# Kernel optimization log

Measured on AMD Instinct MI355X. Metric: run time of the kernel, lower is better.

The kernel has to match this reference:

```python
import jax, jax.numpy as jnp
import numpy as np


def _conv1x1(x, w, b):
    # x: (B,C,H,W), w: (O,C), b: (O,)
    return jnp.einsum('oc,bchw->bohw', w, x) + b[None, :, None, None]


def _avg_pool2(x):
    B, C, H, W = x.shape
    return x.reshape(B, C, H // 2, 2, W // 2, 2).mean(axis=(3, 5))


def setup_inputs() -> dict:
    key = jax.random.key(0)
    B, C, H, W = 8, 64, 64, 64
    ks = jax.random.split(key, 14)
    s = 1.0 / np.sqrt(C)

    def wb(k1, k2):
        return (jax.random.uniform(k1, (C, C), jnp.float32, -s, s),
                jax.random.uniform(k2, (C,), jnp.float32, -s, s))

    w_q, b_q = wb(ks[0], ks[1])
    w_K, b_K = wb(ks[2], ks[3])
    w_V, b_V = wb(ks[4], ks[5])
    w_Q, b_Q = wb(ks[6], ks[7])
    w_k, b_k = wb(ks[8], ks[9])
    w_v, b_v = wb(ks[10], ks[11])
    x = jax.random.normal(ks[12], (B, C, H, W), jnp.float32)
    gamma = jnp.ones((1,), jnp.float32)
    return dict(x=x, w_q=w_q, b_q=b_q, w_K=w_K, b_K=b_K, w_V=w_V, b_V=b_V,
                w_Q=w_Q, b_Q=b_Q, w_k=w_k, b_k=b_k, w_v=w_v, b_v=b_v,
                gamma=gamma)


def reference(x, w_q, b_q, w_K, b_K, w_V, b_V, w_Q, b_Q, w_k, b_k, w_v, b_v, gamma):
    B, C, H, W = x.shape
    N = H * W
    N4 = N // 4

    # Stage 1: pooled queries vs full key/value
    q = _conv1x1(x, w_q, b_q)                      # (B,C,H,W); torch views as (B,C,W,H) but H==W
    qp = _avg_pool2(q).reshape(B, C, N4).transpose(0, 2, 1)   # (B,N/4,C)
    Kf = _conv1x1(x, w_K, b_K).reshape(B, C, N)                # (B,C,N)
    Vf = _conv1x1(x, w_V, b_V).reshape(B, C, N)                # (B,C,N)
    attn = jax.nn.softmax(jnp.einsum('bnc,bcm->bnm', qp, Kf), axis=-1)  # (B,N/4,N)
    out = jnp.einsum('bcm,bnm->bcn', Vf, attn)                 # (B,C,N/4)
    out = out.reshape(B, C, H // 2, W // 2)

    # Stage 2: full queries vs pooled-derived key/value
    Qf = _conv1x1(x, w_Q, b_Q).reshape(B, C, N).transpose(0, 2, 1)  # (B,N,C)
    kp = _conv1x1(out, w_k, b_k).reshape(B, C, N4)                  # (B,C,N/4)
    vp = _conv1x1(out, w_v, b_v).reshape(B, C, N4)                  # (B,C,N/4)
    attn2 = jax.nn.softmax(jnp.einsum('bnc,bcm->bnm', Qf, kp), axis=-1)  # (B,N,N/4)
    out2 = jnp.einsum('bcm,bnm->bcn', vp, attn2).reshape(B, C, H, W)

    return gamma * out2 + x
```

## Files before the change

kernel.cpp:

```cpp
#include <hip/hip_runtime.h>
#include <math.h>


typedef __bf16 bf16;
typedef __attribute__((ext_vector_type(4))) __bf16 bf16x4;
typedef __attribute__((ext_vector_type(8))) __bf16 bf16x8;
typedef __attribute__((ext_vector_type(4))) float f32x4;

constexpr float LOG2E = 1.4426950408889634f;

__device__ __forceinline__ void gl_lds16(const bf16* g, bf16* l) {
    __builtin_amdgcn_global_load_lds(
        (const __attribute__((address_space(1))) unsigned int*)g,
        (__attribute__((address_space(3))) unsigned int*)l,
        16, 0, 0);
}

__device__ __forceinline__ float vexp2(float x) {
    float r;
    asm("v_exp_f32 %0, %1" : "=v"(r) : "v"(x));
    return r;
}
__device__ __forceinline__ unsigned cvtpk(float a, float b) {
    unsigned r;
    asm("v_cvt_pk_bf16_f32 %0, %1, %2" : "=v"(r) : "v"(a), "v"(b));
    return r;
}
__device__ __forceinline__ void swap32(unsigned &a, unsigned &b) {
    asm("v_permlane32_swap_b32 %0, %1" : "+v"(a), "+v"(b));
}
__device__ __forceinline__ void swap16(unsigned &a, unsigned &b) {
    asm("v_permlane16_swap_b32 %0, %1" : "+v"(a), "+v"(b));
}

struct WFrag { bf16x8 f[4][2]; };

template<int WT>
__device__ __forceinline__ WFrag load_wfrag(const float* __restrict__ W, int lane,
                                            float sc = 1.0f) {
    const int c16 = lane & 15, q4 = lane >> 4;
    WFrag wf;
    #pragma unroll
    for (int to = 0; to < 4; ++to)
        #pragma unroll
        for (int h = 0; h < 2; ++h) {
            bf16 tmp[8];
            if (WT == 0) {
                const float* wp = W + (16 * to + c16) * 64 + q4 * 8 + 32 * h;
                float4 f0 = *(const float4*)wp;
                float4 f1 = *(const float4*)(wp + 4);
                tmp[0] = (bf16)(f0.x * sc); tmp[1] = (bf16)(f0.y * sc);
                tmp[2] = (bf16)(f0.z * sc); tmp[3] = (bf16)(f0.w * sc);
                tmp[4] = (bf16)(f1.x * sc); tmp[5] = (bf16)(f1.y * sc);
                tmp[6] = (bf16)(f1.z * sc); tmp[7] = (bf16)(f1.w * sc);
            } else {
                #pragma unroll
                for (int j = 0; j < 8; ++j)
                    tmp[j] = (bf16)(W[(q4 * 8 + 32 * h + j) * 64 + 16 * to + c16] * sc);
            }
            wf.f[to][h] = *(bf16x8*)tmp;
        }
    return wf;
}

template<int OUT>
__device__ __forceinline__ void proj_run(
    const bf16* __restrict__ src, int TN, const WFrag& wf, const float* __restrict__ Bs,
    bf16* __restrict__ Y, int N, int b, int gn0, bf16* __restrict__ Yl, int lane)
{
    const int c16 = lane & 15, q4 = lane >> 4;
    for (int tn = 0; tn < TN; ++tn) {
        bf16x8 xb0 = *(const bf16x8*)&src[(16 * tn + c16) * 72 + q4 * 8];
        bf16x8 xb1 = *(const bf16x8*)&src[(16 * tn + c16) * 72 + q4 * 8 + 32];
        #pragma unroll
        for (int to = 0; to < 4; ++to) {
            f32x4 acc = (f32x4){0.f, 0.f, 0.f, 0.f};
            acc = __builtin_amdgcn_mfma_f32_16x16x32_bf16(wf.f[to][0], xb0, acc, 0, 0, 0);
            acc = __builtin_amdgcn_mfma_f32_16x16x32_bf16(wf.f[to][1], xb1, acc, 0, 0, 0);
            float bias[4] = {0.f, 0.f, 0.f, 0.f};
            if (Bs) {
                float4 b4 = *(const float4*)(Bs + 16 * to + q4 * 4);
                bias[0] = b4.x; bias[1] = b4.y; bias[2] = b4.z; bias[3] = b4.w;
            }
            if (OUT == 0) {
                bf16x4 yv;
                #pragma unroll
                for (int r = 0; r < 4; ++r) yv[r] = (bf16)(acc[r] + bias[r]);
                *(bf16x4*)(Y + ((size_t)b * N + gn0 + 16 * tn + c16) * 64 + 16 * to + 4 * q4) = yv;
            } else if (OUT == 1) {
                #pragma unroll
                for (int r = 0; r < 4; ++r)
                    Y[((size_t)b * 64 + 16 * to + 4 * q4 + r) * N + gn0 + 16 * tn + c16] =
                        (bf16)(acc[r] + bias[r]);
            } else {
                bf16x4 yv;
                #pragma unroll
                for (int r = 0; r < 4; ++r) yv[r] = (bf16)(acc[r] + bias[r]);
                *(bf16x4*)&Yl[(16 * tn + c16) * 72 + 16 * to + 4 * q4] = yv;
            }
        }
    }
}

__global__ __launch_bounds__(256) void prep_kernel(
    const float* __restrict__ x,
    const float* __restrict__ w_q, const float* __restrict__ b_q,
    const float* __restrict__ w_K,
    bf16* __restrict__ xt, bf16* __restrict__ xn, bf16* __restrict__ qkt)
{
    __shared__ float tile[128 * 65];
    __shared__ __align__(16) bf16 xpb[32 * 72];
    __shared__ __align__(16) bf16 qtile[32 * 72];
    const int t  = threadIdx.x;
    const int h2 = blockIdx.x;
    const int b  = blockIdx.y;
    const int n0 = h2 * 128;

    #pragma unroll
    for (int i = 0; i < 32; ++i) {
        int lin = i * 256 + t;
        int n = lin & 127, c = lin >> 7;
        tile[n * 65 + c] = x[((size_t)b * 64 + c) * 4096 + n0 + n];
    }
    __syncthreads();
    {
        int wp = t & 31, c0 = (t >> 5) * 8;
        bf16 tmp[8];
        #pragma unroll
        for (int j = 0; j < 8; ++j) {
            float a = tile[(2 * wp) * 65 + c0 + j] + tile[(2 * wp + 1) * 65 + c0 + j]
                    + tile[(64 + 2 * wp) * 65 + c0 + j] + tile[(64 + 2 * wp + 1) * 65 + c0 + j];
            tmp[j] = (bf16)(0.25f * a);
        }
        *(bf16x8*)&xpb[wp * 72 + c0] = *(bf16x8*)tmp;
    }
    __syncthreads();

    #pragma unroll
    for (int i = 0; i < 4; ++i) {
        int slot = i * 256 + t;
        int n = slot >> 3, c0 = (slot & 7) * 8;
        bf16 tmp[8];
        #pragma unroll
        for (int j = 0; j < 8; ++j) tmp[j] = (bf16)tile[n * 65 + c0 + j];
        *(bf16x8*)&xt[((size_t)b * 4096 + n0 + n) * 64 + c0] = *(bf16x8*)tmp;
    }
    #pragma unroll
    for (int i = 0; i < 4; ++i) {
        int slot = i * 256 + t;
        int c = slot >> 4, n8 = slot & 15;
        bf16 tmp[8];
        #pragma unroll
        for (int j = 0; j < 8; ++j) tmp[j] = (bf16)tile[(n8 * 8 + j) * 65 + c];
        *(bf16x8*)&xn[((size_t)b * 64 + c) * 4096 + n0 + n8 * 8] = *(bf16x8*)tmp;
    }
    if ((t >> 6) == 3) {
        const int lane = t & 63;
        WFrag wfq  = load_wfrag<0>(w_q, lane);
        WFrag wfKT = load_wfrag<1>(w_K, lane, LOG2E);
        proj_run<2>(xpb, 2, wfq, b_q, nullptr, 0, 0, 0, qtile, lane);
        asm volatile("s_waitcnt lgkmcnt(0)" ::: "memory");
        proj_run<0>(qtile, 2, wfKT, nullptr, qkt, 1024, b, h2 * 32, nullptr, lane);
    }
}

template<int NSPLIT, int MODE, int U, int KS, bool BIAS>
__global__ __launch_bounds__(256 * KS, KS == 1 ? 3 : 2) void flash_kernel(
    const bf16* __restrict__ Qt, const bf16* __restrict__ Kt,
    const bf16* __restrict__ Vn, int NQ, int L,
    bf16* __restrict__ Opart, float* __restrict__ Lbuf,
    float* __restrict__ out_f, const float* __restrict__ resid,
    const float* __restrict__ gamma_p, const float* __restrict__ Gb)
{
    const int tid  = threadIdx.x;
    const int lane = tid & 63;
    const int w    = tid >> 6;
    const int wl   = w & 3;
    const int g    = w >> 2;
    const int c16  = lane & 15;
    const int q4   = lane >> 4;
    const int b    = blockIdx.y;
    const int n0   = blockIdx.x * (64 * U) + wl * (16 * U);
    const int s    = (NSPLIT > 1) ? blockIdx.z : 0;
    const int SL   = L / (NSPLIT * KS);
    const int k0   = (s * KS + g) * SL;
    const int ntiles = SL / 64;

    __shared__ __align__(16) char smem[(size_t)KS * 2 * 4096 * 2 * 2];
    bf16* Ksm = (bf16*)smem;
    bf16* Vsm = (bf16*)(smem + (size_t)KS * 2 * 4096 * 2);

    const int rl8 = lane >> 3;
    const int cg  = ((lane & 7) - rl8) & 7;

    const bf16* Kb = Kt + (size_t)b * L * 64;
    const bf16* Vb = Vn + (size_t)b * 64 * L;

    bf16x8 bq[U][2];
    #pragma unroll
    for (int u = 0; u < U; ++u) {
        const bf16* qrow = Qt + ((size_t)b * NQ + n0 + 16 * u + c16) * 64 + q4 * 8;
        bq[u][0] = *(const bf16x8*)(qrow);
        bq[u][1] = *(const bf16x8*)(qrow + 32);
    }

    f32x4 O[U][4];
    #pragma unroll
    for (int u = 0; u < U; ++u)
        #pragma unroll
        for (int gi = 0; gi < 4; ++gi) O[u][gi] = (f32x4){0.f, 0.f, 0.f, 0.f};
    float l_acc[U];
    #pragma unroll
    for (int u = 0; u < U; ++u) l_acc[u] = 0.f;

    #pragma unroll
    for (int j = 0; j < 2; ++j) {
        const int row = 16 * wl + 8 * j + rl8;
        gl_lds16(Kb + (size_t)(k0 + row) * 64 + cg * 8, &Ksm[(g * 2 + 0) * 4096 + (16 * wl + 8 * j) * 64]);
        gl_lds16(Vb + (size_t)row * L + k0 + cg * 8,    &Vsm[(g * 2 + 0) * 4096 + (16 * wl + 8 * j) * 64]);
    }
    __syncthreads();

    for (int it = 0; it < ntiles; ++it) {
        const int buf = it & 1;
        if (it + 1 < ntiles) {
            const int kn = k0 + (it + 1) * 64;
            #pragma unroll
            for (int j = 0; j < 2; ++j) {
                const int row = 16 * wl + 8 * j + rl8;
                gl_lds16(Kb + (size_t)(kn + row) * 64 + cg * 8,
                         &Ksm[(g * 2 + (buf ^ 1)) * 4096 + (16 * wl + 8 * j) * 64]);
                gl_lds16(Vb + (size_t)row * L + kn + cg * 8,
                         &Vsm[(g * 2 + (buf ^ 1)) * 4096 + (16 * wl + 8 * j) * 64]);
            }
        }

        f32x4 sv[U][4];
        #pragma unroll
        for (int t = 0; t < 4; ++t) {
            const bf16* krow = &Ksm[(g * 2 + buf) * 4096 + (16 * t + c16) * 64];
            bf16x8 ak0 = *(const bf16x8*)&krow[((q4 + c16) & 7) * 8];
            bf16x8 ak1 = *(const bf16x8*)&krow[((q4 + 4 + c16) & 7) * 8];
            #pragma unroll
            for (int u = 0; u < U; ++u) {
                f32x4 z = (f32x4){0.f, 0.f, 0.f, 0.f};
                z = __builtin_amdgcn_mfma_f32_16x16x32_bf16(ak0, bq[u][0], z, 0, 0, 0);
                sv[u][t] = __builtin_amdgcn_mfma_f32_16x16x32_bf16(ak1, bq[u][1], z, 0, 0, 0);
            }
        }

        float4 gb[4];
        if (BIAS) {
            #pragma unroll
            for (int t = 0; t < 4; ++t)
                gb[t] = *(const float4*)&Gb[(size_t)b * 1024 + k0 + it * 64 + 16 * t + 4 * q4];
        }

        bf16x8 pfs[U][2];
        #pragma unroll
        for (int u = 0; u < U; ++u) {
            #pragma unroll
            for (int t = 0; t < 4; ++t)
                #pragma unroll
                for (int r = 0; r < 4; ++r) {
                    float sval = sv[u][t][r];
                    if (BIAS) sval += ((const float*)&gb[t])[r];
                    float p = vexp2(sval);
                    sv[u][t][r] = p;
                    l_acc[u] += p;
                }
            unsigned A0 = cvtpk(sv[u][0][0], sv[u][0][1]);
            unsigned A1 = cvtpk(sv[u][0][2], sv[u][0][3]);
            unsigned A2 = cvtpk(sv[u][2][0], sv[u][2][1]);
            unsigned A3 = cvtpk(sv[u][2][2], sv[u][2][3]);
            unsigned B0 = cvtpk(sv[u][1][0], sv[u][1][1]);
            unsigned B1 = cvtpk(sv[u][1][2], sv[u][1][3]);
            unsigned B2 = cvtpk(sv[u][3][0], sv[u][3][1]);
            unsigned B3 = cvtpk(sv[u][3][2], sv[u][3][3]);
            swap32(A0, B0); swap16(A0, B0);
            swap32(A1, B1); swap16(A1, B1);
            swap32(A2, B2); swap16(A2, B2);
            swap32(A3, B3); swap16(A3, B3);
            union { unsigned wd[4]; bf16x8 v; } p0, p1;
            p0.wd[0] = A0; p0.wd[1] = A1; p0.wd[2] = B0; p0.wd[3] = B1;
            p1.wd[0] = A2; p1.wd[1] = A3; p1.wd[2] = B2; p1.wd[3] = B3;
            pfs[u][0] = p0.v;
            pfs[u][1] = p1.v;
        }

        #pragma unroll
        for (int h = 0; h < 2; ++h) {
            #pragma unroll
            for (int gi = 0; gi < 4; ++gi) {
                bf16x8 av = *(const bf16x8*)&Vsm[(g * 2 + buf) * 4096 +
                                                 (16 * gi + c16) * 64 + ((4 * h + q4 + c16) & 7) * 8];
                #pragma unroll
                for (int u = 0; u < U; ++u)
                    O[u][gi] = __builtin_amdgcn_mfma_f32_16x16x32_bf16(av, pfs[u][h], O[u][gi], 0, 0, 0);
            }
        }
        __syncthreads();
    }

    float l_tot[U];
    #pragma unroll
    for (int u = 0; u < U; ++u) {
        float l = l_acc[u];
        l += __shfl_xor(l, 16);
        l += __shfl_xor(l, 32);
        l_tot[u] = l;
    }

    if (KS == 2) {
        float* sc = (float*)smem;
        const int base = (wl * 64 + lane) * 34;
        if (g == 1) {
            #pragma unroll
            for (int u = 0; u < U; ++u) {
                #pragma unroll
                for (int gi = 0; gi < 4; ++gi)
                    #pragma unroll
                    for (int r = 0; r < 4; ++r)
                        sc[base + u * 16 + gi * 4 + r] = O[u][gi][r];
                sc[base + 32 + u] = l_tot[u];
            }
        }
        __syncthreads();
        if (g == 1) return;
        #pragma unroll
        for (int u = 0; u < U; ++u) {
            #pragma unroll
            for (int gi = 0; gi < 4; ++gi)
                #pragma unroll
                for (int r = 0; r < 4; ++r)
                    O[u][gi][r] += sc[base + u * 16 + gi * 4 + r];
            l_tot[u] += sc[base + 32 + u];
        }
    }

    if (MODE == 2) {
        const float gm = gamma_p[0];
        #pragma unroll
        for (int u = 0; u < U; ++u) {
            float inv = gm / l_tot[u];
            const int n = n0 + 16 * u + c16;
            #pragma unroll
            for (int gi = 0; gi < 4; ++gi) {
                #pragma unroll
                for (int r = 0; r < 4; ++r) {
                    size_t oidx = ((size_t)b * 64 + 16 * gi + 4 * q4 + r) * NQ + n;
                    out_f[oidx] = O[u][gi][r] * inv + resid[oidx];
                }
            }
        }
    } else {
        #pragma unroll
        for (int u = 0; u < U; ++u) {
            float inv = 1.0f / l_tot[u];
            bf16* dst = Opart + ((size_t)(b * NSPLIT + s) * NQ + n0 + 16 * u + c16) * 64 + q4 * 4;
            #pragma unroll
            for (int gi = 0; gi < 4; ++gi) {
                bf16x4 yv;
                #pragma unroll
                for (int r = 0; r < 4; ++r) yv[r] = (bf16)(O[u][gi][r] * inv);
                *(bf16x4*)(dst + 16 * gi) = yv;
            }
        }
        if (lane < 16) {
            #pragma unroll
            for (int u = 0; u < U; ++u)
                Lbuf[(b * NSPLIT + s) * NQ + n0 + 16 * u + lane] = l_tot[u];
        }
    }
}

__global__ __launch_bounds__(256) void comb1kv_kernel(
    const bf16* __restrict__ Opart, const float* __restrict__ Lbuf,
    const float* __restrict__ w_V, const float* __restrict__ b_V,
    const float* __restrict__ w_k, const float* __restrict__ b_k,
    const float* __restrict__ w_v, const float* __restrict__ b_v,
    const float* __restrict__ w_Q, const float* __restrict__ b_Q,
    bf16* __restrict__ qk2t, bf16* __restrict__ vp, float* __restrict__ Gb)
{
    constexpr int NS = 4;
    __shared__ __align__(16) bf16 tile[32 * 72];
    __shared__ __align__(16) bf16 otile[32 * 72];
    __shared__ __align__(16) bf16 kpl[32 * 72];
    __shared__ float wbuf[32 * NS];
    const int t  = threadIdx.x;
    const int m0 = blockIdx.x * 32;
    const int b  = blockIdx.y;
    const int w  = t >> 6;
    const int lane = t & 63;

    WFrag wf;
    if      (w == 0) wf = load_wfrag<0>(w_V, lane);
    else if (w == 1) wf = load_wfrag<0>(w_k, lane);
    else if (w == 2) wf = load_wfrag<0>(w_v, lane);
    else             wf = load_wfrag<1>(w_Q, lane, LOG2E);

    if (t < 32) {
        int m = m0 + t;
        float ls[NS], lt = 0.f;
        #pragma unroll
        for (int s = 0; s < NS; ++s) {
            ls[s] = Lbuf[(b * NS + s) * 1024 + m];
            lt += ls[s];
        }
        float inv = 1.f / lt;
        #pragma unroll
        for (int s = 0; s < NS; ++s) wbuf[t * NS + s] = ls[s] * inv;
    }
    __syncthreads();

    #pragma unroll
    for (int i = 0; i < 2; ++i) {
        int ml = i * 16 + (t >> 4);
        int c4 = (t & 15) * 4;
        const bf16* base = Opart + ((size_t)(b * NS) * 1024 + m0 + ml) * 64 + c4;
        float a0 = 0.f, a1 = 0.f, a2 = 0.f, a3 = 0.f;
        #pragma unroll
        for (int s = 0; s < NS; ++s) {
            bf16x4 v = *(const bf16x4*)(base + (size_t)s * 1024 * 64);
            float wg = wbuf[ml * NS + s];
            a0 += (float)v[0] * wg; a1 += (float)v[1] * wg;
            a2 += (float)v[2] * wg; a3 += (float)v[3] * wg;
        }
        bf16x4 o; o[0] = (bf16)a0; o[1] = (bf16)a1; o[2] = (bf16)a2; o[3] = (bf16)a3;
        *(bf16x4*)&tile[ml * 72 + c4] = o;
    }
    __syncthreads();

    if (w == 0) proj_run<2>(tile, 2, wf, b_V, nullptr, 0, 0, 0, otile, lane);
    __syncthreads();
    if (w == 1) proj_run<2>(otile, 2, wf, b_k, nullptr, 0, 0, 0, kpl, lane);
    if (w == 2) proj_run<1>(otile, 2, wf, b_v, vp, 1024, b, m0, nullptr, lane);
    __syncthreads();
    if (w == 3) proj_run<0>(kpl, 2, wf, nullptr, qk2t, 1024, b, m0, nullptr, lane);
    if (w == 0 && lane < 32) {
        float acc = 0.f;
        #pragma unroll
        for (int c = 0; c < 64; ++c) acc += b_Q[c] * (float)kpl[lane * 72 + c];
        Gb[(size_t)b * 1024 + m0 + lane] = acc * LOG2E;
    }
}

extern "C" void kernel_launch(void* const* d_in, const int* in_sizes, int n_in,
                              void* d_out, int out_size, void* d_ws, size_t ws_size,
                              hipStream_t stream) {
    const float* x    = (const float*)d_in[0];
    const float* w_q  = (const float*)d_in[1];
    const float* b_q  = (const float*)d_in[2];
    const float* w_K  = (const float*)d_in[3];
    const float* b_K  = (const float*)d_in[4];   (void)b_K;
    const float* w_V  = (const float*)d_in[5];
    const float* b_V  = (const float*)d_in[6];
    const float* w_Q  = (const float*)d_in[7];
    const float* b_Q  = (const float*)d_in[8];
    const float* w_k  = (const float*)d_in[9];
    const float* b_k  = (const float*)d_in[10];
    const float* w_v  = (const float*)d_in[11];
    const float* b_v  = (const float*)d_in[12];
    const float* gamma = (const float*)d_in[13];
    float* out = (float*)d_out;

    char* ws = (char*)d_ws;
    bf16*  xt    = (bf16*)ws;   ws += (size_t)8 * 4096 * 64 * 2;
    bf16*  xn    = (bf16*)ws;   ws += (size_t)8 * 4096 * 64 * 2;
    bf16*  qkt   = (bf16*)ws;   ws += (size_t)8 * 1024 * 64 * 2;
    bf16*  qk2t  = (bf16*)ws;   ws += (size_t)8 * 1024 * 64 * 2;
    bf16*  vp    = (bf16*)ws;   ws += (size_t)8 * 64 * 1024 * 2;
    bf16*  Opart = (bf16*)ws;   ws += (size_t)8 * 4 * 1024 * 64 * 2;
    float* Lb    = (float*)ws;  ws += (size_t)8 * 4 * 1024 * 4;
    float* Gb    = (float*)ws;  ws += (size_t)8 * 1024 * 4;

    prep_kernel<<<dim3(32, 8), 256, 0, stream>>>(x, w_q, b_q, w_K, xt, xn, qkt);

    flash_kernel<4, 1, 2, 2, false><<<dim3(8, 8, 4), 512, 0, stream>>>(
        qkt, xt, xn, 1024, 4096, Opart, Lb, nullptr, nullptr, nullptr, nullptr);

    comb1kv_kernel<<<dim3(32, 8), 256, 0, stream>>>(
        Opart, Lb, w_V, b_V, w_k, b_k, w_v, b_v, w_Q, b_Q, qk2t, vp, Gb);

    flash_kernel<1, 2, 2, 2, true><<<dim3(32, 8, 1), 512, 0, stream>>>(
        xt, qk2t, vp, 4096, 1024, nullptr, nullptr, out, x, gamma, Gb);
}
```

Before: 133.4 us.

## Fuse four pipeline kernels into one cooperative persistent kernel with grid syncs

The four launches (prep, first flash attention, combine/projection, second flash attention) are merged into one cooperative kernel of 256 blocks × 512 threads, with grid-wide barriers between phases. Each phase is now a device function working on one shared 64 KB shared-memory buffer, and the prep and combine phases are adapted to the 512-thread block. The aim is to remove per-launch overhead and the idle gaps between dependent kernels. The trade-off is the cost of grid.sync barriers, a single fused register allocation sized for the heaviest phase, and one block per CU.

Result: slower. 229.8 us (+72.3%).

```diff
diff --git a/kernel.cpp b/kernel.cpp
--- a/kernel.cpp
+++ b/kernel.cpp
@@ -1,5 +1,8 @@
 #include <hip/hip_runtime.h>
+#include <hip/hip_cooperative_groups.h>
 #include <math.h>
+
+namespace cg = cooperative_groups;
 
 
 typedef __bf16 bf16;
@@ -102,28 +105,26 @@
     }
 }
 
-__global__ __launch_bounds__(256) void prep_kernel(
+__device__ __forceinline__ void prep_phase(
+    char* smem, int t, int h2, int b,
     const float* __restrict__ x,
     const float* __restrict__ w_q, const float* __restrict__ b_q,
     const float* __restrict__ w_K,
     bf16* __restrict__ xt, bf16* __restrict__ xn, bf16* __restrict__ qkt)
 {
-    __shared__ float tile[128 * 65];
-    __shared__ __align__(16) bf16 xpb[32 * 72];
-    __shared__ __align__(16) bf16 qtile[32 * 72];
-    const int t  = threadIdx.x;
-    const int h2 = blockIdx.x;
-    const int b  = blockIdx.y;
+    float* tile = (float*)smem;
+    bf16* xpb   = (bf16*)(smem + 33280);
+    bf16* qtile = (bf16*)(smem + 37888);
     const int n0 = h2 * 128;
 
     #pragma unroll
-    for (int i = 0; i < 32; ++i) {
-        int lin = i * 256 + t;
+    for (int i = 0; i < 16; ++i) {
+        int lin = i * 512 + t;
         int n = lin & 127, c = lin >> 7;
         tile[n * 65 + c] = x[((size_t)b * 64 + c) * 4096 + n0 + n];
     }
     __syncthreads();
-    {
+    if (t < 256) {
         int wp = t & 31, c0 = (t >> 5) * 8;
         bf16 tmp[8];
         #pragma unroll
@@ -137,8 +138,8 @@
     __syncthreads();
 
     #pragma unroll
-    for (int i = 0; i < 4; ++i) {
-        int slot = i * 256 + t;
+    for (int i = 0; i < 2; ++i) {
+        int slot = i * 512 + t;
         int n = slot >> 3, c0 = (slot & 7) * 8;
         bf16 tmp[8];
         #pragma unroll
@@ -146,8 +147,8 @@
         *(bf16x8*)&xt[((size_t)b * 4096 + n0 + n) * 64 + c0] = *(bf16x8*)tmp;
     }
     #pragma unroll
-    for (int i = 0; i < 4; ++i) {
-        int slot = i * 256 + t;
+    for (int i = 0; i < 2; ++i) {
+        int slot = i * 512 + t;
         int c = slot >> 4, n8 = slot & 15;
         bf16 tmp[8];
         #pragma unroll
@@ -164,31 +165,29 @@
     }
 }
 
-template<int NSPLIT, int MODE, int U, int KS, bool BIAS>
-__global__ __launch_bounds__(256 * KS, KS == 1 ? 3 : 2) void flash_kernel(
+template<int NSPLIT, int MODE, int U, bool BIAS>
+__device__ __forceinline__ void flash_phase(
+    char* smem, int tid, int bx, int b, int s,
     const bf16* __restrict__ Qt, const bf16* __restrict__ Kt,
     const bf16* __restrict__ Vn, int NQ, int L,
     bf16* __restrict__ Opart, float* __restrict__ Lbuf,
     float* __restrict__ out_f, const float* __restrict__ resid,
     const float* __restrict__ gamma_p, const float* __restrict__ Gb)
 {
-    const int tid  = threadIdx.x;
+    constexpr int KS = 2;
     const int lane = tid & 63;
     const int w    = tid >> 6;
     const int wl   = w & 3;
     const int g    = w >> 2;
     const int c16  = lane & 15;
     const int q4   = lane >> 4;
-    const int b    = blockIdx.y;
-    const int n0   = blockIdx.x * (64 * U) + wl * (16 * U);
-    const int s    = (NSPLIT > 1) ? blockIdx.z : 0;
+    const int n0   = bx * (64 * U) + wl * (16 * U);
     const int SL   = L / (NSPLIT * KS);
     const int k0   = (s * KS + g) * SL;
     const int ntiles = SL / 64;
 
-    __shared__ __align__(16) char smem[(size_t)KS * 2 * 4096 * 2 * 2];
     bf16* Ksm = (bf16*)smem;
-    bf16* Vsm = (bf16*)(smem + (size_t)KS * 2 * 4096 * 2);
+    bf16* Vsm = (bf16*)(smem + 32768);
 
     const int rl8 = lane >> 3;
     const int cg  = ((lane & 7) - rl8) & 7;
@@ -311,7 +310,7 @@
         l_tot[u] = l;
     }
 
-    if (KS == 2) {
+    {
         float* sc = (float*)smem;
         const int base = (wl * 64 + lane) * 34;
         if (g == 1) {
@@ -326,55 +325,59 @@
             }
         }
         __syncthreads();
-        if (g == 1) return;
-        #pragma unroll
-        for (int u = 0; u < U; ++u) {
-            #pragma unroll
-            for (int gi = 0; gi < 4; ++gi)
-                #pragma unroll
-                for (int r = 0; r < 4; ++r)
-                    O[u][gi][r] += sc[base + u * 16 + gi * 4 + r];
-            l_tot[u] += sc[base + 32 + u];
-        }
-    }
-
-    if (MODE == 2) {
-        const float gm = gamma_p[0];
-        #pragma unroll
-        for (int u = 0; u < U; ++u) {
-            float inv = gm / l_tot[u];
-            const int n = n0 + 16 * u + c16;
-            #pragma unroll
-            for (int gi = 0; gi < 4; ++gi) {
-                #pragma unroll
-                for (int r = 0; r < 4; ++r) {
-                    size_t oidx = ((size_t)b * 64 + 16 * gi + 4 * q4 + r) * NQ + n;
-                    out_f[oidx] = O[u][gi][r] * inv + resid[oidx];
+        if (g == 0) {
+            #pragma unroll
+            for (int u = 0; u < U; ++u) {
+                #pragma unroll
+                for (int gi = 0; gi < 4; ++gi)
+                    #pragma unroll
+                    for (int r = 0; r < 4; ++r)
+                        O[u][gi][r] += sc[base + u * 16 + gi * 4 + r];
+                l_tot[u] += sc[base + 32 + u];
+            }
+        }
+    }
+
+    if (g == 0) {
+        if (MODE == 2) {
+            const float gm = gamma_p[0];
+            #pragma unroll
+            for (int u = 0; u < U; ++u) {
+                float inv = gm / l_tot[u];
+                const int n = n0 + 16 * u + c16;
+                #pragma unroll
+                for (int gi = 0; gi < 4; ++gi) {
+                    #pragma unroll
+                    for (int r = 0; r < 4; ++r) {
+                        size_t oidx = ((size_t)b * 64 + 16 * gi + 4 * q4 + r) * NQ + n;
+                        out_f[oidx] = O[u][gi][r] * inv + resid[oidx];
+                    }
                 }
             }
-        }
-    } else {
-        #pragma unroll
-        for (int u = 0; u < U; ++u) {
-            float inv = 1.0f / l_tot[u];
-            bf16* dst = Opart + ((size_t)(b * NSPLIT + s) * NQ + n0 + 16 * u + c16) * 64 + q4 * 4;
-            #pragma unroll
-            for (int gi = 0; gi < 4; ++gi) {
-                bf16x4 yv;
-                #pragma unroll
-                for (int r = 0; r < 4; ++r) yv[r] = (bf16)(O[u][gi][r] * inv);
-                *(bf16x4*)(dst + 16 * gi) = yv;
-            }
-        }
-        if (lane < 16) {
-            #pragma unroll
-            for (int u = 0; u < U; ++u)
-                Lbuf[(b * NSPLIT + s) * NQ + n0 + 16 * u + lane] = l_tot[u];
-        }
-    }
-}
-
-__global__ __launch_bounds__(256) void comb1kv_kernel(
+        } else {
+            #pragma unroll
+            for (int u = 0; u < U; ++u) {
+                float inv = 1.0f / l_tot[u];
+                bf16* dst = Opart + ((size_t)(b * NSPLIT + s) * NQ + n0 + 16 * u + c16) * 64 + q4 * 4;
+                #pragma unroll
+                for (int gi = 0; gi < 4; ++gi) {
+                    bf16x4 yv;
+                    #pragma unroll
+                    for (int r = 0; r < 4; ++r) yv[r] = (bf16)(O[u][gi][r] * inv);
+                    *(bf16x4*)(dst + 16 * gi) = yv;
+                }
+            }
+            if (lane < 16) {
+                #pragma unroll
+                for (int u = 0; u < U; ++u)
+                    Lbuf[(b * NSPLIT + s) * NQ + n0 + 16 * u + lane] = l_tot[u];
+            }
+        }
+    }
+}
+
+__device__ __forceinline__ void comb_phase(
+    char* smem, int t, int m0, int b,
     const bf16* __restrict__ Opart, const float* __restrict__ Lbuf,
     const float* __restrict__ w_V, const float* __restrict__ b_V,
     const float* __restrict__ w_k, const float* __restrict__ b_k,
@@ -383,13 +386,10 @@
     bf16* __restrict__ qk2t, bf16* __restrict__ vp, float* __restrict__ Gb)
 {
     constexpr int NS = 4;
-    __shared__ __align__(16) bf16 tile[32 * 72];
-    __shared__ __align__(16) bf16 otile[32 * 72];
-    __shared__ __align__(16) bf16 kpl[32 * 72];
-    __shared__ float wbuf[32 * NS];
-    const int t  = threadIdx.x;
-    const int m0 = blockIdx.x * 32;
-    const int b  = blockIdx.y;
+    bf16* tile  = (bf16*)smem;
+    bf16* otile = (bf16*)(smem + 4608);
+    bf16* kpl   = (bf16*)(smem + 9216);
+    float* wbuf = (float*)(smem + 13824);
     const int w  = t >> 6;
     const int lane = t & 63;
 
@@ -397,7 +397,7 @@
     if      (w == 0) wf = load_wfrag<0>(w_V, lane);
     else if (w == 1) wf = load_wfrag<0>(w_k, lane);
     else if (w == 2) wf = load_wfrag<0>(w_v, lane);
-    else             wf = load_wfrag<1>(w_Q, lane, LOG2E);
+    else if (w == 3) wf = load_wfrag<1>(w_Q, lane, LOG2E);
 
     if (t < 32) {
         int m = m0 + t;
@@ -413,9 +413,8 @@
     }
     __syncthreads();
 
-    #pragma unroll
-    for (int i = 0; i < 2; ++i) {
-        int ml = i * 16 + (t >> 4);
+    {
+        int ml = t >> 4;
         int c4 = (t & 15) * 4;
         const bf16* base = Opart + ((size_t)(b * NS) * 1024 + m0 + ml) * 64 + c4;
         float a0 = 0.f, a1 = 0.f, a2 = 0.f, a3 = 0.f;
@@ -443,6 +442,41 @@
         for (int c = 0; c < 64; ++c) acc += b_Q[c] * (float)kpl[lane * 72 + c];
         Gb[(size_t)b * 1024 + m0 + lane] = acc * LOG2E;
     }
+}
+
+__global__ __launch_bounds__(512, 1) void fused_kernel(
+    const float* __restrict__ x,
+    const float* __restrict__ w_q, const float* __restrict__ b_q,
+    const float* __restrict__ w_K,
+    const float* __restrict__ w_V, const float* __restrict__ b_V,
+    const float* __restrict__ w_Q, const float* __restrict__ b_Q,
+    const float* __restrict__ w_k, const float* __restrict__ b_k,
+    const float* __restrict__ w_v, const float* __restrict__ b_v,
+    const float* __restrict__ gamma_p, float* __restrict__ out,
+    bf16* __restrict__ xt, bf16* __restrict__ xn,
+    bf16* __restrict__ qkt, bf16* __restrict__ qk2t, bf16* __restrict__ vp,
+    bf16* __restrict__ Opart, float* __restrict__ Lb, float* __restrict__ Gb)
+{
+    __shared__ __align__(16) char smem[65536];
+    cg::grid_group grid = cg::this_grid();
+    const int bid = blockIdx.x;
+    const int tid = threadIdx.x;
+
+    prep_phase(smem, tid, bid & 31, bid >> 5, x, w_q, b_q, w_K, xt, xn, qkt);
+    grid.sync();
+
+    flash_phase<4, 1, 2, false>(smem, tid, bid & 7, (bid >> 3) & 7, bid >> 6,
+                                qkt, xt, xn, 1024, 4096,
+                                Opart, Lb, nullptr, nullptr, nullptr, nullptr);
+    grid.sync();
+
+    comb_phase(smem, tid, (bid & 31) * 32, bid >> 5, Opart, Lb,
+               w_V, b_V, w_k, b_k, w_v, b_v, w_Q, b_Q, qk2t, vp, Gb);
+    grid.sync();
+
+    flash_phase<1, 2, 2, true>(smem, tid, bid & 31, bid >> 5, 0,
+                               xt, qk2t, vp, 4096, 1024,
+                               nullptr, nullptr, out, x, gamma_p, Gb);
 }
 
 extern "C" void kernel_launch(void* const* d_in, const int* in_sizes, int n_in,
@@ -474,14 +508,14 @@
     float* Lb    = (float*)ws;  ws += (size_t)8 * 4 * 1024 * 4;
     float* Gb    = (float*)ws;  ws += (size_t)8 * 1024 * 4;
 
-    prep_kernel<<<dim3(32, 8), 256, 0, stream>>>(x, w_q, b_q, w_K, xt, xn, qkt);
-
-    flash_kernel<4, 1, 2, 2, false><<<dim3(8, 8, 4), 512, 0, stream>>>(
-        qkt, xt, xn, 1024, 4096, Opart, Lb, nullptr, nullptr, nullptr, nullptr);
-
-    comb1kv_kernel<<<dim3(32, 8), 256, 0, stream>>>(
-        Opart, Lb, w_V, b_V, w_k, b_k, w_v, b_v, w_Q, b_Q, qk2t, vp, Gb);
-
-    flash_kernel<1, 2, 2, 2, true><<<dim3(32, 8, 1), 512, 0, stream>>>(
-        xt, qk2t, vp, 4096, 1024, nullptr, nullptr, out, x, gamma, Gb);
-}
+    void* args[] = {
+        (void*)&x, (void*)&w_q, (void*)&b_q, (void*)&w_K,
+        (void*)&w_V, (void*)&b_V, (void*)&w_Q, (void*)&b_Q,
+        (void*)&w_k, (void*)&b_k, (void*)&w_v, (void*)&b_v,
+        (void*)&gamma, (void*)&out,
+        (void*)&xt, (void*)&xn, (void*)&qkt, (void*)&qk2t, (void*)&vp,
+        (void*)&Opart, (void*)&Lb, (void*)&Gb
+    };
+    hipLaunchCooperativeKernel((void*)fused_kernel, dim3(256), dim3(512),
+                               args, 0, stream);
+}
```
